# Performance work log

Hardware: AMD Instinct MI355X
Metric: run time of the kernel (lower is better)

The kernel has to match this reference:

```python
import jax, jax.numpy as jnp
import numpy as np

B, N_PER, E_PER = 32, 2048, 4096          # graphs, nodes/graph, edges/graph
NN, NE = B * N_PER, B * E_PER              # 65536 nodes, 131072 edges
F_IN, EMB, H, OUT, VOCAB = 32, 32, 128, 64, 10000


def _glorot(k, shape):
    lim = float(np.sqrt(6.0 / (shape[0] + shape[-1])))
    return jax.random.uniform(k, shape, jnp.float32, -lim, lim)


def setup_inputs() -> dict:
    key = jax.random.key(0)
    ks = jax.random.split(key, 20)
    x = jax.random.normal(ks[0], (NN, F_IN), jnp.float32)
    node_index = jax.random.randint(ks[1], (NN,), 0, VOCAB)
    # intra-graph edges, nodes sorted by graph -> edge batch is sorted too
    off = jnp.repeat(jnp.arange(B) * N_PER, E_PER)
    src = jax.random.randint(ks[2], (NE,), 0, N_PER) + off
    dst = jax.random.randint(ks[3], (NE,), 0, N_PER) + off
    edge_index = jnp.stack([src, dst])
    d_in = F_IN + EMB
    return dict(
        x=x, node_index=node_index, edge_index=edge_index,
        emb=jax.random.normal(ks[4], (VOCAB, EMB), jnp.float32),
        W1=_glorot(ks[5], (d_in, H)), a1s=_glorot(ks[6], (H,)), a1d=_glorot(ks[7], (H,)), b1=jnp.zeros((H,), jnp.float32),
        W2=_glorot(ks[8], (H, H)),   a2s=_glorot(ks[9], (H,)), a2d=_glorot(ks[10], (H,)), b2=jnp.zeros((H,), jnp.float32),
        W3=_glorot(ks[11], (H, H)),  a3s=_glorot(ks[12], (H,)), a3d=_glorot(ks[13], (H,)), b3=jnp.zeros((H,), jnp.float32),
        fcW=_glorot(ks[14], (2 * H, H)), fcb=jnp.zeros((H,), jnp.float32),
        Wz=_glorot(ks[15], (H + OUT, OUT)), bz=jnp.zeros((OUT,), jnp.float32),
        Wr=_glorot(ks[16], (H + OUT, OUT)), br=jnp.zeros((OUT,), jnp.float32),
        Wh=_glorot(ks[17], (H + OUT, OUT)), bh=jnp.zeros((OUT,), jnp.float32),
    )


def _gat(h_in, W, a_s, a_d, b, src, dst):
    # single-head GATConv with self-loops already appended to (src, dst)
    h = h_in @ W                                              # [NN, H]
    e = jax.nn.leaky_relu((h @ a_s)[src] + (h @ a_d)[dst], 0.2)  # [E']
    m = jax.ops.segment_max(e, dst, num_segments=NN)
    ex = jnp.exp(e - m[dst])
    s = jax.ops.segment_sum(ex, dst, num_segments=NN)
    alpha = ex / s[dst]
    return jax.ops.segment_sum(h[src] * alpha[:, None], dst, num_segments=NN) + b


def reference(x, node_index, edge_index, emb, W1, a1s, a1d, b1, W2, a2s, a2d, b2,
              W3, a3s, a3d, b3, fcW, fcb, Wz, bz, Wr, br, Wh, bh):
    gelu = lambda v: jax.nn.gelu(v, approximate=False)  # torch F.gelu default = erf
    h = jnp.concatenate([x, emb[node_index]], axis=1)   # [NN, F_IN+EMB]
    loops = jnp.arange(NN)
    src = jnp.concatenate([edge_index[0], loops])
    dst = jnp.concatenate([edge_index[1], loops])
    h = gelu(_gat(h, W1, a1s, a1d, b1, src, dst))
    h = gelu(_gat(h, W2, a2s, a2d, b2, src, dst))
    h = gelu(_gat(h, W3, a3s, a3d, b3, src, dst))
    # per-edge features (original edges, no self-loops)
    ef = jnp.concatenate([h[edge_index[0]], h[edge_index[1]]], axis=-1)  # [NE, 2H]
    ef = gelu(ef @ fcW + fcb)                                            # [NE, H]
    # equal-size graphs, edges sorted by graph -> construct_tensor == reshape, mask all-ones
    gru_in = ef.reshape(B, E_PER, H).transpose(1, 0, 2)                  # [T, B, H]

    def step(hid, xt):
        c = jnp.concatenate([xt, hid], axis=1)
        z = jax.nn.sigmoid(c @ Wz + bz)
        r = jax.nn.sigmoid(c @ Wr + br)
        cr = jnp.concatenate([xt, r * hid], axis=1)
        ht = jax.nn.leaky_relu(cr @ Wh + bh, 0.01)
        return (1 - z) * hid + z * ht, None

    hid, _ = jax.lax.scan(step, jnp.zeros((B, OUT), ef.dtype), gru_in)
    # predict_graph=True with all-ones mask -> prediction at last timestep == final hidden
    return hid
```

## Files before the change

kernel.cpp:

```cpp
#include <hip/hip_runtime.h>
#include <hip/hip_bf16.h>
#include <math.h>

#define NN_ 65536
#define NE_ 131072
#define B_  32
#define T_  4096

__device__ __forceinline__ float gelu_f(float x){
    return 0.5f*x*(1.0f + erff(x*0.70710678118654752f));
}

__device__ __forceinline__ unsigned enc_f(float f){
    unsigned b = __float_as_uint(f);
    return (b & 0x80000000u) ? ~b : (b | 0x80000000u);
}
__device__ __forceinline__ float dec_f(unsigned u){
    return (u & 0x80000000u) ? __uint_as_float(u ^ 0x80000000u) : __uint_as_float(~u);
}

__device__ __forceinline__ float rdlane(float v, int l){
    return __int_as_float(__builtin_amdgcn_readlane(__float_as_int(v), l));
}

__global__ void k_zero(float* p, int n){
    int i = blockIdx.x*blockDim.x + threadIdx.x;
    int stride = gridDim.x*blockDim.x;
    for(; i<n; i+=stride) p[i] = 0.f;
}

__global__ void k_embed(const float* __restrict__ x, const int* __restrict__ nidx,
                        const float* __restrict__ emb, float* __restrict__ h64){
    int gid = blockIdx.x*256 + threadIdx.x;
    int n = gid >> 6, c = gid & 63;
    float v = (c < 32) ? x[(size_t)n*32 + c] : emb[(size_t)nidx[n]*32 + (c-32)];
    h64[gid] = v;
}

template<int K>
__global__ void k_gemm_node(const float* __restrict__ A, const float* __restrict__ W,
                            float* __restrict__ C){
    int lane = threadIdx.x & 63;
    int wy = threadIdx.x >> 6;
    int r0 = blockIdx.x*16 + wy*4;
    const float* a0 = A + (size_t)r0*K;
    float acc0[4] = {0,0,0,0}, acc1[4] = {0,0,0,0};
    #pragma unroll 4
    for(int k=0;k<K;k+=4){
        float4 av[4];
        #pragma unroll
        for(int i=0;i<4;i++) av[i] = *(const float4*)(a0 + (size_t)i*K + k);
        #pragma unroll
        for(int kk=0;kk<4;kk++){
            float w0 = W[(size_t)(k+kk)*128 + lane];
            float w1 = W[(size_t)(k+kk)*128 + 64 + lane];
            #pragma unroll
            for(int i=0;i<4;i++){
                float a = ((const float*)&av[i])[kk];
                acc0[i] += a*w0;
                acc1[i] += a*w1;
            }
        }
    }
    #pragma unroll
    for(int i=0;i<4;i++){
        C[(size_t)(r0+i)*128 + lane]      = acc0[i];
        C[(size_t)(r0+i)*128 + 64 + lane] = acc1[i];
    }
}

__global__ void k_rowdots(const float* __restrict__ hW, const float* __restrict__ as_,
                          const float* __restrict__ ad_, float* __restrict__ ssrc,
                          float* __restrict__ sdst){
    int lane = threadIdx.x & 63;
    int row = blockIdx.x*4 + (threadIdx.x >> 6);
    const float* hp = hW + (size_t)row*128;
    float h0 = hp[lane], h1 = hp[lane+64];
    float d0 = h0*as_[lane] + h1*as_[lane+64];
    float d1 = h0*ad_[lane] + h1*ad_[lane+64];
    #pragma unroll
    for(int off=32; off; off>>=1){
        d0 += __shfl_xor(d0, off);
        d1 += __shfl_xor(d1, off);
    }
    if(lane==0){ ssrc[row] = d0; sdst[row] = d1; }
}

__global__ void k_edge1(const int* __restrict__ src, const int* __restrict__ dst,
                        const float* __restrict__ ssrc, const float* __restrict__ sdst,
                        float* __restrict__ ebuf, unsigned* __restrict__ menc){
    int e = blockIdx.x*256 + threadIdx.x;
    int s, d;
    if(e < NE_){ s = src[e]; d = dst[e]; } else { s = d = e - NE_; }
    float v = ssrc[s] + sdst[d];
    v = (v > 0.f) ? v : 0.2f*v;
    ebuf[e] = v;
    atomicMax(&menc[d], enc_f(v));
}

__global__ void k_edge2(const int* __restrict__ dst, const unsigned* __restrict__ menc,
                        float* __restrict__ ebuf, float* __restrict__ ssum){
    int e = blockIdx.x*256 + threadIdx.x;
    int d = (e < NE_) ? dst[e] : (e - NE_);
    float m = dec_f(menc[d]);
    float ex = __expf(ebuf[e] - m);
    ebuf[e] = ex;
    atomicAdd(&ssum[d], ex);
}

__global__ void __launch_bounds__(256) k_edge3_lds(
        const int* __restrict__ src, const int* __restrict__ dst,
        const float* __restrict__ ebuf, const float* __restrict__ ssum,
        const float* __restrict__ hW, const float* __restrict__ bias,
        float* __restrict__ hAgg){
    __shared__ float agg[2048][8];
    int g  = blockIdx.x;
    int c0 = blockIdx.y << 3;
    int t  = threadIdx.x;
    int cc = t & 7;
    int elane = t >> 3;

    for(int idx = t; idx < 2048*8; idx += 256)
        ((float*)agg)[idx] = 0.f;
    __syncthreads();

    const int gbase_e = g << 12;
    const int gbase_n = g << 11;
    for(int i = 0; i < 192; i++){
        int eg = i*32 + elane;
        int s, dloc; float a;
        if(eg < 4096){
            int e = gbase_e + eg;
            s    = src[e];
            int d = dst[e];
            dloc = d - gbase_n;
            a    = ebuf[e] / ssum[d];
        } else {
            int nl = eg - 4096;
            s    = gbase_n + nl;
            dloc = nl;
            a    = ebuf[NE_ + gbase_n + nl] / ssum[gbase_n + nl];
        }
        float v = hW[(size_t)s*128 + c0 + cc] * a;
        atomicAdd(&agg[dloc][cc], v);
    }
    __syncthreads();

    for(int idx = t; idx < 2048*8; idx += 256){
        int nl = idx >> 3;
        int ch = c0 + (idx & 7);
        hAgg[((size_t)(gbase_n + nl))*128 + ch] = gelu_f(agg[nl][idx & 7] + bias[ch]);
    }
}

__global__ void k_ef_x3(const float* __restrict__ h3, const int* __restrict__ src,
                        const int* __restrict__ dst, const float* __restrict__ fcW,
                        const float* __restrict__ fcb,
                        const float* __restrict__ Wz, const float* __restrict__ Wr,
                        const float* __restrict__ Wh, const float* __restrict__ bz,
                        const float* __restrict__ br, const float* __restrict__ bh,
                        float* __restrict__ X3){
    __shared__ float efs[16][128];
    int lane = threadIdx.x & 63;
    int wy = threadIdx.x >> 6;
    int e0 = blockIdx.x*16 + wy*4;

    {
        float acc0[4] = {0,0,0,0}, acc1[4] = {0,0,0,0};
        #pragma unroll
        for(int half=0; half<2; half++){
            const float* rowp[4];
            #pragma unroll
            for(int i=0;i<4;i++){
                int n = (half==0) ? src[e0+i] : dst[e0+i];
                rowp[i] = h3 + (size_t)n*128;
            }
            #pragma unroll 2
            for(int k=0;k<128;k+=4){
                float4 av[4];
                #pragma unroll
                for(int i=0;i<4;i++) av[i] = *(const float4*)(rowp[i] + k);
                #pragma unroll
                for(int kk=0;kk<4;kk++){
                    int kw = half*128 + k + kk;
                    float w0 = fcW[(size_t)kw*128 + lane];
                    float w1 = fcW[(size_t)kw*128 + 64 + lane];
                    #pragma unroll
                    for(int i=0;i<4;i++){
                        float a = ((const float*)&av[i])[kk];
                        acc0[i] += a*w0;
                        acc1[i] += a*w1;
                    }
                }
            }
        }
        float b0 = fcb[lane], b1 = fcb[64+lane];
        #pragma unroll
        for(int i=0;i<4;i++){
            efs[wy*4+i][lane]      = gelu_f(acc0[i] + b0);
            efs[wy*4+i][64 + lane] = gelu_f(acc1[i] + b1);
        }
    }
    __syncthreads();
    {
        float accz[4] = {0,0,0,0}, accr[4] = {0,0,0,0}, acch[4] = {0,0,0,0};
        #pragma unroll 2
        for(int k=0;k<128;k+=4){
            #pragma unroll
            for(int kk=0;kk<4;kk++){
                float w0 = Wz[(size_t)(k+kk)*64 + lane];
                float w1 = Wr[(size_t)(k+kk)*64 + lane];
                float w2 = Wh[(size_t)(k+kk)*64 + lane];
                #pragma unroll
                for(int i=0;i<4;i++){
                    float a = efs[wy*4+i][k+kk];
                    accz[i] += a*w0;
                    accr[i] += a*w1;
                    acch[i] += a*w2;
                }
            }
        }
        float b0 = bz[lane], b1 = br[lane], b2 = bh[lane];
        #pragma unroll
        for(int i=0;i<4;i++){
            int e = e0 + i;
            int bb = e >> 12;
            int t  = e & 4095;
            float* o = X3 + ((size_t)t*32 + bb)*192;
            o[lane]       = accz[i] + b0;
            o[64 + lane]  = accr[i] + b1;
            o[128 + lane] = acch[i] + b2;
        }
    }
}

__global__ void __launch_bounds__(256) k_gru(const float* __restrict__ X3,
                       const float* __restrict__ Wz, const float* __restrict__ Wr,
                       const float* __restrict__ Wh, float* __restrict__ out){
    __shared__ float2 P1[4][64];
    __shared__ float  P2[4][64];
    int b = blockIdx.x;
    int j = threadIdx.x & 63;
    int w = __builtin_amdgcn_readfirstlane(threadIdx.x >> 6);
    int kbase = w << 4;

    float wz[16], wr[16], wh[16];
    #pragma unroll
    for(int i=0;i<16;i++){
        wz[i] = Wz[(size_t)(128+kbase+i)*64 + j];
        wr[i] = Wr[(size_t)(128+kbase+i)*64 + j];
        wh[i] = Wh[(size_t)(128+kbase+i)*64 + j];
    }

    float h = 0.f;
    const float* x0 = X3 + (size_t)b*192;
    float xz = x0[j], xr = x0[64+j], xh = x0[128+j];

    for(int step=0; step<T_; step++){
        float nxz, nxr, nxh;
        if(step + 1 < T_){
            const float* np = X3 + ((size_t)(step+1)*32 + b)*192;
            nxz = np[j]; nxr = np[64+j]; nxh = np[128+j];
        } else { nxz = nxr = nxh = 0.f; }

        float az0=0.f, az1=0.f, ar0=0.f, ar1=0.f;
        #pragma unroll
        for(int i=0;i<16;i+=2){
            float h0 = rdlane(h, kbase+i);
            float h1 = rdlane(h, kbase+i+1);
            az0 = fmaf(h0, wz[i],   az0); ar0 = fmaf(h0, wr[i],   ar0);
            az1 = fmaf(h1, wz[i+1], az1); ar1 = fmaf(h1, wr[i+1], ar1);
        }
        P1[w][j] = make_float2(az0+az1, ar0+ar1);
        __syncthreads();
        float2 p0 = P1[0][j], p1 = P1[1][j], p2 = P1[2][j], p3 = P1[3][j];
        float sz = xz + ((p0.x+p1.x)+(p2.x+p3.x));
        float sr = xr + ((p0.y+p1.y)+(p2.y+p3.y));
        float z = 1.f/(1.f + __expf(-sz));
        float r = 1.f/(1.f + __expf(-sr));
        float rh = r*h;

        float ah0=0.f, ah1=0.f;
        #pragma unroll
        for(int i=0;i<16;i+=2){
            float r0 = rdlane(rh, kbase+i);
            float r1 = rdlane(rh, kbase+i+1);
            ah0 = fmaf(r0, wh[i],   ah0);
            ah1 = fmaf(r1, wh[i+1], ah1);
        }
        P2[w][j] = ah0+ah1;
        __syncthreads();
        float s2 = xh + ((P2[0][j]+P2[1][j]) + (P2[2][j]+P2[3][j]));
        float ht = (s2 > 0.f) ? s2 : 0.01f*s2;

        h = (1.f - z)*h + z*ht;
        xz = nxz; xr = nxr; xh = nxh;
    }
    if(w == 0) out[(size_t)b*64 + j] = h;
}

extern "C" void kernel_launch(void* const* d_in, const int* in_sizes, int n_in,
                              void* d_out, int out_size, void* d_ws, size_t ws_size,
                              hipStream_t stream) {
    const float* x    = (const float*)d_in[0];
    const int*   nidx = (const int*)d_in[1];
    const int*   src  = (const int*)d_in[2];
    const int*   dst  = src + NE_;
    const float* emb  = (const float*)d_in[3];
    const float* W1 = (const float*)d_in[4];
    const float* a1s = (const float*)d_in[5];
    const float* a1d = (const float*)d_in[6];
    const float* b1 = (const float*)d_in[7];
    const float* W2 = (const float*)d_in[8];
    const float* a2s = (const float*)d_in[9];
    const float* a2d = (const float*)d_in[10];
    const float* b2 = (const float*)d_in[11];
    const float* W3 = (const float*)d_in[12];
    const float* a3s = (const float*)d_in[13];
    const float* a3d = (const float*)d_in[14];
    const float* b3 = (const float*)d_in[15];
    const float* fcW = (const float*)d_in[16];
    const float* fcb = (const float*)d_in[17];
    const float* Wz = (const float*)d_in[18];
    const float* bz = (const float*)d_in[19];
    const float* Wr = (const float*)d_in[20];
    const float* br = (const float*)d_in[21];
    const float* Wh = (const float*)d_in[22];
    const float* bh = (const float*)d_in[23];
    float* out = (float*)d_out;

    float* ws = (float*)d_ws;
    float* hAgg = ws;
    float* X3   = hAgg + (size_t)NN_*128;
    float* bufA = X3;
    float* h64  = bufA + (size_t)NN_*128;
    float* ssrc = h64  + (size_t)NN_*64;
    float* sdst = ssrc + NN_;
    float* ssum = sdst + NN_;
    unsigned* menc = (unsigned*)(ssum + NN_);
    float* ebuf = (float*)menc + NN_;

    const int EP = NE_ + NN_;

    k_embed<<<NN_*64/256, 256, 0, stream>>>(x, nidx, emb, h64);

    const float* Ws[3]  = {W1, W2, W3};
    const float* as_[3] = {a1s, a2s, a3s};
    const float* ad_[3] = {a1d, a2d, a3d};
    const float* bs[3]  = {b1, b2, b3};

    for(int l=0; l<3; l++){
        if(l == 0)
            k_gemm_node<64><<<NN_/16, 256, 0, stream>>>(h64, Ws[l], bufA);
        else
            k_gemm_node<128><<<NN_/16, 256, 0, stream>>>(hAgg, Ws[l], bufA);
        k_zero<<<512, 256, 0, stream>>>(ssum, 2*NN_);
        k_rowdots<<<NN_/4, 256, 0, stream>>>(bufA, as_[l], ad_[l], ssrc, sdst);
        k_edge1<<<EP/256, 256, 0, stream>>>(src, dst, ssrc, sdst, ebuf, menc);
        k_edge2<<<EP/256, 256, 0, stream>>>(dst, menc, ebuf, ssum);
        k_edge3_lds<<<dim3(B_, 16), 256, 0, stream>>>(src, dst, ebuf, ssum, bufA, bs[l], hAgg);
    }

    k_ef_x3<<<NE_/16, 256, 0, stream>>>(hAgg, src, dst, fcW, fcb,
                                        Wz, Wr, Wh, bz, br, bh, X3);
    k_gru<<<B_, 256, 0, stream>>>(X3, Wz, Wr, Wh, out);
}
```

Before: 3.768 ms.

## Run GRU recurrence in a single wavefront with packed fp16 dot2 weights

```diff
diff --git a/kernel.cpp b/kernel.cpp
--- a/kernel.cpp
+++ b/kernel.cpp
@@ -7,6 +7,8 @@
 #define B_  32
 #define T_  4096
 
+typedef __fp16 f16x2 __attribute__((ext_vector_type(2)));
+
 __device__ __forceinline__ float gelu_f(float x){
     return 0.5f*x*(1.0f + erff(x*0.70710678118654752f));
 }
@@ -21,6 +23,19 @@
 
 __device__ __forceinline__ float rdlane(float v, int l){
     return __int_as_float(__builtin_amdgcn_readlane(__float_as_int(v), l));
+}
+__device__ __forceinline__ int rdlane_i(int v, int l){
+    return __builtin_amdgcn_readlane(v, l);
+}
+__device__ __forceinline__ int h2i(f16x2 h){ union{int i; f16x2 h;} u; u.h=h; return u.i; }
+__device__ __forceinline__ f16x2 i2h(int i){ union{int i; f16x2 h;} u; u.i=i; return u.h; }
+
+__device__ __forceinline__ float dot2(f16x2 a, f16x2 b, float c){
+#if __has_builtin(__builtin_amdgcn_fdot2)
+    return __builtin_amdgcn_fdot2(a, b, c, false);
+#else
+    return c + (float)a.x*(float)b.x + (float)a.y*(float)b.y;
+#endif
 }
 
 __global__ void k_zero(float* p, int n){
@@ -234,69 +249,77 @@
     }
 }
 
-__global__ void __launch_bounds__(256) k_gru(const float* __restrict__ X3,
+__global__ void __launch_bounds__(64) k_gru(const float* __restrict__ X3,
                        const float* __restrict__ Wz, const float* __restrict__ Wr,
                        const float* __restrict__ Wh, float* __restrict__ out){
-    __shared__ float2 P1[4][64];
-    __shared__ float  P2[4][64];
     int b = blockIdx.x;
-    int j = threadIdx.x & 63;
-    int w = __builtin_amdgcn_readfirstlane(threadIdx.x >> 6);
-    int kbase = w << 4;
-
-    float wz[16], wr[16], wh[16];
+    int j = threadIdx.x;
+    int odd = j & 1;
+
+    f16x2 wzp[32], wrp[32], whp[32];
     #pragma unroll
-    for(int i=0;i<16;i++){
-        wz[i] = Wz[(size_t)(128+kbase+i)*64 + j];
-        wr[i] = Wr[(size_t)(128+kbase+i)*64 + j];
-        wh[i] = Wh[(size_t)(128+kbase+i)*64 + j];
+    for(int i=0;i<32;i++){
+        wzp[i] = __builtin_amdgcn_cvt_pkrtz(Wz[(size_t)(128+2*i)*64 + j], Wz[(size_t)(128+2*i+1)*64 + j]);
+        wrp[i] = __builtin_amdgcn_cvt_pkrtz(Wr[(size_t)(128+2*i)*64 + j], Wr[(size_t)(128+2*i+1)*64 + j]);
+        whp[i] = __builtin_amdgcn_cvt_pkrtz(Wh[(size_t)(128+2*i)*64 + j], Wh[(size_t)(128+2*i+1)*64 + j]);
     }
 
     float h = 0.f;
-    const float* x0 = X3 + (size_t)b*192;
-    float xz = x0[j], xr = x0[64+j], xh = x0[128+j];
+    const float* p0 = X3 + (size_t)b*192;
+    float xz = p0[j], xr = p0[64+j], xh = p0[128+j];
+    const float* p1 = X3 + ((size_t)32 + b)*192;
+    float n1z = p1[j], n1r = p1[64+j], n1h = p1[128+j];
 
     for(int step=0; step<T_; step++){
-        float nxz, nxr, nxh;
-        if(step + 1 < T_){
-            const float* np = X3 + ((size_t)(step+1)*32 + b)*192;
-            nxz = np[j]; nxr = np[64+j]; nxh = np[128+j];
-        } else { nxz = nxr = nxh = 0.f; }
-
-        float az0=0.f, az1=0.f, ar0=0.f, ar1=0.f;
-        #pragma unroll
-        for(int i=0;i<16;i+=2){
-            float h0 = rdlane(h, kbase+i);
-            float h1 = rdlane(h, kbase+i+1);
-            az0 = fmaf(h0, wz[i],   az0); ar0 = fmaf(h0, wr[i],   ar0);
-            az1 = fmaf(h1, wz[i+1], az1); ar1 = fmaf(h1, wr[i+1], ar1);
-        }
-        P1[w][j] = make_float2(az0+az1, ar0+ar1);
-        __syncthreads();
-        float2 p0 = P1[0][j], p1 = P1[1][j], p2 = P1[2][j], p3 = P1[3][j];
-        float sz = xz + ((p0.x+p1.x)+(p2.x+p3.x));
-        float sr = xr + ((p0.y+p1.y)+(p2.y+p3.y));
-        float z = 1.f/(1.f + __expf(-sz));
-        float r = 1.f/(1.f + __expf(-sr));
+        float n2z, n2r, n2h;
+        if(step + 2 < T_){
+            const float* p2 = X3 + ((size_t)(step+2)*32 + b)*192;
+            n2z = p2[j]; n2r = p2[64+j]; n2h = p2[128+j];
+        } else { n2z = n2r = n2h = 0.f; }
+
+        float hn = __shfl_xor(h, 1);
+        int hp = h2i(__builtin_amdgcn_cvt_pkrtz(odd ? hn : h, odd ? h : hn));
+
+        float az0 = xz, az1 = 0.f, az2 = 0.f, az3 = 0.f;
+        float ar0 = xr, ar1 = 0.f, ar2 = 0.f, ar3 = 0.f;
+        #pragma unroll
+        for(int i=0;i<32;i+=4){
+            f16x2 h0 = i2h(rdlane_i(hp, 2*i));
+            f16x2 h1 = i2h(rdlane_i(hp, 2*i+2));
+            f16x2 h2 = i2h(rdlane_i(hp, 2*i+4));
+            f16x2 h3 = i2h(rdlane_i(hp, 2*i+6));
+            az0 = dot2(h0, wzp[i],   az0); ar0 = dot2(h0, wrp[i],   ar0);
+            az1 = dot2(h1, wzp[i+1], az1); ar1 = dot2(h1, wrp[i+1], ar1);
+            az2 = dot2(h2, wzp[i+2], az2); ar2 = dot2(h2, wrp[i+2], ar2);
+            az3 = dot2(h3, wzp[i+3], az3); ar3 = dot2(h3, wrp[i+3], ar3);
+        }
+        float z = 1.f/(1.f + __expf(-((az0+az1)+(az2+az3))));
+        float r = 1.f/(1.f + __expf(-((ar0+ar1)+(ar2+ar3))));
         float rh = r*h;
 
-        float ah0=0.f, ah1=0.f;
-        #pragma unroll
-        for(int i=0;i<16;i+=2){
-            float r0 = rdlane(rh, kbase+i);
-            float r1 = rdlane(rh, kbase+i+1);
-            ah0 = fmaf(r0, wh[i],   ah0);
-            ah1 = fmaf(r1, wh[i+1], ah1);
-        }
-        P2[w][j] = ah0+ah1;
-        __syncthreads();
-        float s2 = xh + ((P2[0][j]+P2[1][j]) + (P2[2][j]+P2[3][j]));
-        float ht = (s2 > 0.f) ? s2 : 0.01f*s2;
-
-        h = (1.f - z)*h + z*ht;
-        xz = nxz; xr = nxr; xh = nxh;
-    }
-    if(w == 0) out[(size_t)b*64 + j] = h;
+        float rn = __shfl_xor(rh, 1);
+        int rp = h2i(__builtin_amdgcn_cvt_pkrtz(odd ? rn : rh, odd ? rh : rn));
+
+        float ah0 = xh, ah1 = 0.f, ah2 = 0.f, ah3 = 0.f;
+        #pragma unroll
+        for(int i=0;i<32;i+=4){
+            f16x2 r0 = i2h(rdlane_i(rp, 2*i));
+            f16x2 r1 = i2h(rdlane_i(rp, 2*i+2));
+            f16x2 r2 = i2h(rdlane_i(rp, 2*i+4));
+            f16x2 r3 = i2h(rdlane_i(rp, 2*i+6));
+            ah0 = dot2(r0, whp[i],   ah0);
+            ah1 = dot2(r1, whp[i+1], ah1);
+            ah2 = dot2(r2, whp[i+2], ah2);
+            ah3 = dot2(r3, whp[i+3], ah3);
+        }
+        float s2 = (ah0+ah1)+(ah2+ah3);
+        float ht = fmaxf(s2, 0.01f*s2);
+
+        h = fmaf(z, ht - h, h);
+        xz = n1z; xr = n1r; xh = n1h;
+        n1z = n2z; n1r = n2r; n1h = n2h;
+    }
+    out[(size_t)b*64 + j] = h;
 }
 
 extern "C" void kernel_launch(void* const* d_in, const int* in_sizes, int n_in,
@@ -363,5 +386,5 @@
 
     k_ef_x3<<<NE_/16, 256, 0, stream>>>(hAgg, src, dst, fcW, fcb,
                                         Wz, Wr, Wh, bz, br, bh, X3);
-    k_gru<<<B_, 256, 0, stream>>>(X3, Wz, Wr, Wh, out);
-}
+    k_gru<<<B_, 64, 0, stream>>>(X3, Wz, Wr, Wh, out);
+}
```

Result: slower. 4.464 ms (+18.5%).
